# Optimization experiments

Measured on AMD Instinct MI355X. Metric: run time of the kernel, lower is better.

## Reference

```python
import jax, jax.numpy as jnp
import numpy as np

EPS = 1e-7
MIN_NORM = 1e-15
PROJ_EPS = 4e-3
C = 1.0
HEADS = 4
NEG_SLOPE = 0.2

def artanh(x):
    x = jnp.clip(x, -1.0 + EPS, 1.0 - EPS)
    return 0.5 * (jnp.log1p(x) - jnp.log1p(-x))

def _norm(x):
    return jnp.clip(jnp.linalg.norm(x, axis=-1, keepdims=True), MIN_NORM)

def proj(x, c):
    n = _norm(x)
    maxnorm = (1.0 - PROJ_EPS) / jnp.sqrt(c)
    return jnp.where(n > maxnorm, x / n * maxnorm, x)

def expmap0(u, c):
    sc = jnp.sqrt(c)
    n = _norm(u)
    return jnp.tanh(sc * n) * u / (sc * n)

def logmap0(p, c):
    sc = jnp.sqrt(c)
    n = _norm(p)
    return artanh(sc * n) * p / (sc * n)

def mobius_add(x, y, c):
    x2 = jnp.sum(x * x, -1, keepdims=True)
    y2 = jnp.sum(y * y, -1, keepdims=True)
    xy = jnp.sum(x * y, -1, keepdims=True)
    num = (1 + 2 * c * xy + c * y2) * x + (1 - c * x2) * y
    den = 1 + 2 * c * xy + c * c * x2 * y2
    return num / jnp.clip(den, MIN_NORM)

def mobius_matvec(m, x, c):
    sc = jnp.sqrt(c)
    xn = _norm(x)
    mx = x @ m.T
    mxn = _norm(mx)
    res = jnp.tanh(mxn / xn * artanh(sc * xn)) * mx / (mxn * sc)
    zero = jnp.all(mx == 0, axis=-1, keepdims=True)
    return jnp.where(zero, 0.0, res)

def segment_softmax(scores, seg, n):
    # scores: [E, H], seg: [E] destination node ids
    smax = jax.ops.segment_max(scores, seg, num_segments=n)
    smax = jnp.where(jnp.isfinite(smax), smax, 0.0)
    ex = jnp.exp(scores - smax[seg])
    den = jax.ops.segment_sum(ex, seg, num_segments=n)
    return ex / jnp.clip(den[seg], MIN_NORM)


def setup_inputs() -> dict:
    key = jax.random.key(0)
    ks = jax.random.split(key, 6)
    N, D_IN, D_OUT, E = 50000, 128, 128, 800000
    x = 0.01 * jax.random.normal(ks[0], (N, D_IN), dtype=jnp.float32)
    W = (math := np.sqrt(2.0 * 6.0 / (D_IN + D_OUT))) * jax.random.uniform(ks[1], (D_OUT, D_IN), dtype=jnp.float32, minval=-1.0, maxval=1.0)
    lin_bias = jnp.zeros((D_OUT,), jnp.float32)
    att = 0.1 * jax.random.normal(ks[2], (1, HEADS, 2 * (D_OUT // HEADS)), dtype=jnp.float32)
    conv_bias = jnp.zeros((D_OUT,), jnp.float32)
    src = jax.random.randint(ks[3], (E,), 0, N, dtype=jnp.int32)
    # guarantee no self loops (module removes them before adding canonical ones)
    dst = (src + 1 + jax.random.randint(ks[4], (E,), 0, N - 1, dtype=jnp.int32)) % N
    return {"x": x, "W": W, "lin_bias": lin_bias, "att": att,
            "conv_bias": conv_bias, "edge_src": src, "edge_dst": dst}


def reference(x, W, lin_bias, att, conv_bias, edge_src, edge_dst):
    N = x.shape[0]
    H = HEADS
    # ---- HypLinear (c=1, eval mode so no dropout) ----
    h = proj(mobius_matvec(W, x, C), C)
    hyp_bias = proj(expmap0(lin_bias, C), C)   # proj_tan0 is identity on Poincare ball
    h = proj(mobius_add(h, hyp_bias, C), C)
    D = h.shape[-1] // H
    # ---- add self loops ----
    loops = jnp.arange(N, dtype=edge_src.dtype)
    src = jnp.concatenate([edge_src, loops])   # j (source)
    dst = jnp.concatenate([edge_dst, loops])   # i (target / aggregation index)
    # ---- tangent-space GAT message passing ----
    log_x = logmap0(h, C).reshape(N, H, D)
    x_i = log_x[dst]                            # [E, H, D]
    x_j = log_x[src]                            # [E, H, D]
    att_i, att_j = att[0, :, :D], att[0, :, D:]
    alpha = jnp.einsum('ehd,hd->eh', x_i, att_i) + jnp.einsum('ehd,hd->eh', x_j, att_j)
    alpha = jax.nn.leaky_relu(alpha, NEG_SLOPE)
    alpha = segment_softmax(alpha, dst, N)      # [E, H]
    msg = x_j * alpha[:, :, None]
    out = jax.ops.segment_sum(msg, dst, num_segments=N)  # [N, H, D]
    out = out.reshape(N, H * D) + conv_bias
    # ---- update / activation / map back to manifold ----
    out = jax.nn.relu(out)                      # proj_tan0 is identity
    return proj(expmap0(out, C), C)
```

## Files before the change

kernel.cpp:

```cpp
#include <hip/hip_runtime.h>
#include <hip/hip_fp16.h>
#include <math.h>

#define EPSF 1e-7f
#define MIN_NORM 1e-15f
#define MAXNORM 0.996f
#define NEG_SLOPE 0.2f

typedef __attribute__((ext_vector_type(8))) short short8;
typedef __attribute__((ext_vector_type(4))) float f32x4;

__device__ __forceinline__ float wave_reduce_sum(float v) {
    #pragma unroll
    for (int m = 1; m < 64; m <<= 1) v += __shfl_xor(v, m, 64);
    return v;
}

__device__ __forceinline__ float fast_tanh(float x) {
    float e = __expf(2.f * x);
    return 1.f - 2.f / (e + 1.f);
}

__device__ __forceinline__ float fast_artanh(float x) {
    x = fminf(fmaxf(x, -1.f + EPSF), 1.f - EPSF);
    return 0.5f * __logf((1.f + x) / (1.f - x));
}

__device__ __forceinline__ float lrelu(float a) {
    return a < 0.f ? a * NEG_SLOPE : a;
}

__device__ __forceinline__ unsigned short f2bf(float f) {
    unsigned u = __float_as_uint(f);
    u += 0x7FFFu + ((u >> 16) & 1u);
    return (unsigned short)(u >> 16);
}
__device__ __forceinline__ float bf2f(unsigned short h) {
    return __uint_as_float(((unsigned)h) << 16);
}

__global__ void prep_kernel(const float* __restrict__ W,
                            unsigned short* __restrict__ whi,
                            unsigned short* __restrict__ wlo,
                            const float* __restrict__ lin_bias,
                            float* __restrict__ bbuf,
                            int* __restrict__ head, int headN) {
    if (blockIdx.x >= 65) {
        int i = (blockIdx.x - 65) * 1024 + threadIdx.x * 4;
        if (i < headN) *(int4*)&head[i] = make_int4(-1, -1, -1, -1);
        return;
    }
    if (blockIdx.x == 64) {
        if (threadIdx.x >= 64) return;
        int lane = threadIdx.x;
        float u0 = lin_bias[lane], u1 = lin_bias[lane + 64];
        float n2 = wave_reduce_sum(u0 * u0 + u1 * u1);
        float n = fmaxf(sqrtf(n2), MIN_NORM);
        float s = tanhf(n) / n;
        float b0 = s * u0, b1 = s * u1;
        float bn = fmaxf(tanhf(n), MIN_NORM);
        float fn2 = bn * bn;
        if (bn > MAXNORM) { float f = MAXNORM / bn; b0 *= f; b1 *= f; fn2 = MAXNORM * MAXNORM; }
        bbuf[lane] = b0;
        bbuf[lane + 64] = b1;
        if (lane == 0) bbuf[128] = fn2;
        return;
    }
    int idx = blockIdx.x * 256 + threadIdx.x;
    int i = idx & 7, l = (idx >> 3) & 63, ts = idx >> 9;
    int s = ts & 3, t = ts >> 2;
    int o = t * 16 + (l & 15);
    int k = s * 32 + ((l >> 4) * 8) + i;
    float f = W[o * 128 + k];
    unsigned short h = f2bf(f);
    unsigned short lo = f2bf(f - bf2f(h));
    whi[idx] = h;
    wlo[idx] = lo;
}

#define DPAD 132
__global__ __launch_bounds__(256) void node_kernel(
    const float* __restrict__ x,
    const unsigned short* __restrict__ whi, const unsigned short* __restrict__ wlo,
    const float* __restrict__ bbuf, const float* __restrict__ att,
    unsigned short* __restrict__ log_xb,
    float* __restrict__ s_i, float* __restrict__ s_j, int N)
{
    __shared__ float mxs[16][DPAD];
    __shared__ float xn2s[16];
    int tid = threadIdx.x, wave = tid >> 6, lane = tid & 63;
    int nbase = blockIdx.x * 16;
    int arow = lane & 15, kgrp = lane >> 4;
    int anode = min(nbase + arow, N - 1);

    f32x4 acc0 = {0.f, 0.f, 0.f, 0.f};
    f32x4 acc1 = {0.f, 0.f, 0.f, 0.f};
    int t0 = wave * 2, t1 = wave * 2 + 1;
    float x2loc = 0.f;

    #pragma unroll
    for (int s = 0; s < 4; ++s) {
        const float* xp = x + (size_t)anode * 128 + s * 32 + kgrp * 8;
        float4 xa = *(const float4*)xp;
        float4 xb = *(const float4*)(xp + 4);
        float xv[8] = {xa.x, xa.y, xa.z, xa.w, xb.x, xb.y, xb.z, xb.w};
        short8 ahi, alo;
        #pragma unroll
        for (int i = 0; i < 8; ++i) {
            unsigned short h = f2bf(xv[i]);
            unsigned short l = f2bf(xv[i] - bf2f(h));
            ahi[i] = (short)h;
            alo[i] = (short)l;
        }
        if (wave == 0) {
            #pragma unroll
            for (int i = 0; i < 8; ++i) x2loc = fmaf(xv[i], xv[i], x2loc);
        }
        short8 bh0 = *(const short8*)(whi + ((size_t)(t0 * 4 + s) * 64 + lane) * 8);
        short8 bl0 = *(const short8*)(wlo + ((size_t)(t0 * 4 + s) * 64 + lane) * 8);
        short8 bh1 = *(const short8*)(whi + ((size_t)(t1 * 4 + s) * 64 + lane) * 8);
        short8 bl1 = *(const short8*)(wlo + ((size_t)(t1 * 4 + s) * 64 + lane) * 8);
        acc0 = __builtin_amdgcn_mfma_f32_16x16x32_bf16(ahi, bh0, acc0, 0, 0, 0);
        acc0 = __builtin_amdgcn_mfma_f32_16x16x32_bf16(alo, bh0, acc0, 0, 0, 0);
        acc0 = __builtin_amdgcn_mfma_f32_16x16x32_bf16(ahi, bl0, acc0, 0, 0, 0);
        acc1 = __builtin_amdgcn_mfma_f32_16x16x32_bf16(ahi, bh1, acc1, 0, 0, 0);
        acc1 = __builtin_amdgcn_mfma_f32_16x16x32_bf16(alo, bh1, acc1, 0, 0, 0);
        acc1 = __builtin_amdgcn_mfma_f32_16x16x32_bf16(ahi, bl1, acc1, 0, 0, 0);
    }
    if (wave == 0) {
        x2loc += __shfl_xor(x2loc, 16, 64);
        x2loc += __shfl_xor(x2loc, 32, 64);
        if (lane < 16) xn2s[lane] = x2loc;
    }
    #pragma unroll
    for (int r = 0; r < 4; ++r) {
        mxs[kgrp * 4 + r][t0 * 16 + arow] = acc0[r];
        mxs[kgrp * 4 + r][t1 * 16 + arow] = acc1[r];
    }
    __syncthreads();

    int g16 = lane >> 4, l16 = lane & 15;
    int nn = wave * 4 + g16;
    int node = nbase + nn;
    bool valid = node < N;
    int head = l16 >> 2;
    int dbase = l16 * 8;
    int dd8 = (l16 & 3) * 8;
    float bb[8], aiv[8], ajv[8];
    #pragma unroll
    for (int j = 0; j < 8; ++j) {
        bb[j] = bbuf[dbase + j];
        aiv[j] = att[head * 64 + dd8 + j];
        ajv[j] = att[head * 64 + 32 + dd8 + j];
    }
    float y2 = bbuf[128];

    float4 va = *(const float4*)&mxs[nn][dbase];
    float4 vb = *(const float4*)&mxs[nn][dbase + 4];
    float v[8] = {va.x, va.y, va.z, va.w, vb.x, vb.y, vb.z, vb.w};

    float mq = 0.f;
    #pragma unroll
    for (int j = 0; j < 8; ++j) mq = fmaf(v[j], v[j], mq);
    #pragma unroll
    for (int m = 1; m < 16; m <<= 1) mq += __shfl_xor(mq, m, 64);

    float xn2 = xn2s[nn];
    float xn = fmaxf(sqrtf(xn2), MIN_NORM);
    float mxn = fmaxf(sqrtf(mq), MIN_NORM);
    float t = fast_tanh(mxn / xn * fast_artanh(xn));
    float scl = t / mxn;
    bool zero = (mq == 0.f);
    float r[8];
    #pragma unroll
    for (int j = 0; j < 8; ++j) r[j] = zero ? 0.f : scl * v[j];
    float rn2 = zero ? 0.f : t * t;
    float rn = zero ? MIN_NORM : fmaxf(fabsf(t), MIN_NORM);
    float x2 = rn2;
    if (rn > MAXNORM) {
        float f = MAXNORM / rn;
        #pragma unroll
        for (int j = 0; j < 8; ++j) r[j] *= f;
        x2 = MAXNORM * MAXNORM;
    }
    float xy = 0.f;
    #pragma unroll
    for (int j = 0; j < 8; ++j) xy = fmaf(r[j], bb[j], xy);
    #pragma unroll
    for (int m = 1; m < 16; m <<= 1) xy += __shfl_xor(xy, m, 64);
    float cA = 1.f + 2.f * xy + y2;
    float cB = 1.f - x2;
    float dn = fmaxf(1.f + 2.f * xy + x2 * y2, MIN_NORM);
    float inv = 1.f / dn;
    float h[8];
    #pragma unroll
    for (int j = 0; j < 8; ++j) h[j] = (cA * r[j] + cB * bb[j]) * inv;
    float hq = 0.f;
    #pragma unroll
    for (int j = 0; j < 8; ++j) hq = fmaf(h[j], h[j], hq);
    #pragma unroll
    for (int m = 1; m < 16; m <<= 1) hq += __shfl_xor(hq, m, 64);
    float hn = fmaxf(sqrtf(hq), MIN_NORM);
    float ln2 = hq;
    if (hn > MAXNORM) {
        float f = MAXNORM / hn;
        #pragma unroll
        for (int j = 0; j < 8; ++j) h[j] *= f;
        ln2 = MAXNORM * MAXNORM;
    }
    float lnn = fmaxf(sqrtf(ln2), MIN_NORM);
    float ls = fast_artanh(lnn) / lnn;
    float lv[8];
    #pragma unroll
    for (int j = 0; j < 8; ++j) lv[j] = ls * h[j];

    if (valid) {
        uint4 pk;
        pk.x = (unsigned)f2bf(lv[0]) | ((unsigned)f2bf(lv[1]) << 16);
        pk.y = (unsigned)f2bf(lv[2]) | ((unsigned)f2bf(lv[3]) << 16);
        pk.z = (unsigned)f2bf(lv[4]) | ((unsigned)f2bf(lv[5]) << 16);
        pk.w = (unsigned)f2bf(lv[6]) | ((unsigned)f2bf(lv[7]) << 16);
        *(uint4*)&log_xb[(size_t)node * 128 + dbase] = pk;
    }
    float pi = 0.f, pj = 0.f;
    #pragma unroll
    for (int j = 0; j < 8; ++j) {
        pi = fmaf(lv[j], aiv[j], pi);
        pj = fmaf(lv[j], ajv[j], pj);
    }
    pi += __shfl_xor(pi, 1, 64); pi += __shfl_xor(pi, 2, 64);
    pj += __shfl_xor(pj, 1, 64); pj += __shfl_xor(pj, 2, 64);
    if (valid && (l16 & 3) == 0) {
        int pos = ((head & 1) << 1) | (head >> 1);
        s_i[(size_t)node * 4 + pos] = pi;
        s_j[(size_t)node * 4 + pos] = pj;
    }
}

__global__ void buildw_kernel(const int* __restrict__ src, const int* __restrict__ dst,
                              int E, const float* __restrict__ s_i,
                              const float* __restrict__ s_j,
                              int* __restrict__ head, int4* __restrict__ pair16)
{
    int e = blockIdx.x * blockDim.x + threadIdx.x;
    if (e >= E) return;
    int s_ = src[e], d_ = dst[e];
    int prev = atomicExch(&head[(size_t)d_ * 16 + (e & 15)], e);
    float4 si = *(const float4*)(s_i + (size_t)d_ * 4);
    float4 sj = *(const float4*)(s_j + (size_t)s_ * 4);
    float w0 = __expf(lrelu(si.x + sj.x));
    float w1 = __expf(lrelu(si.y + sj.y));
    float w2 = __expf(lrelu(si.z + sj.z));
    float w3 = __expf(lrelu(si.w + sj.w));
    __half2 h01 = __floats2half2_rn(w0, w1);
    __half2 h23 = __floats2half2_rn(w2, w3);
    int4 pr;
    pr.x = s_ << 8;
    pr.y = prev;
    pr.z = *(int*)&h01;
    pr.w = *(int*)&h23;
    pair16[e] = pr;
}

#define MAXS 128
__global__ __launch_bounds__(256) void aggregate_kernel(
    const int* __restrict__ head, const int4* __restrict__ pair16,
    const float* __restrict__ s_i, const float* __restrict__ s_j,
    const unsigned short* __restrict__ log_xb, const float* __restrict__ conv_bias,
    float* __restrict__ out, int N)
{
    __shared__ __align__(16) int slist[4][MAXS];
    __shared__ __align__(16) unsigned wlist[4][MAXS * 2];
    __shared__ int scnt[4];
    int tid = threadIdx.x, wave = tid >> 6, lane = tid & 63;
    int n = blockIdx.x * 4 + wave;
    bool valid = n < N;

    if (lane == 0) scnt[wave] = 0;
    __syncthreads();

    int resume = -1;
    if (valid && lane < 16) {
        int e = head[(size_t)n * 16 + lane];
        while (e >= 0) {
            int4 pr = pair16[e];
            int pos = atomicAdd(&scnt[wave], 1);
            if (pos < MAXS) {
                slist[wave][pos] = pr.x;
                wlist[wave][pos * 2]     = (unsigned)pr.z;
                wlist[wave][pos * 2 + 1] = (unsigned)pr.w;
                e = pr.y;
            } else { resume = e; break; }
        }
    }
    __syncthreads();

    int g = lane >> 5;
    float acc0 = 0.f, acc1 = 0.f, dna = 0.f, dnb = 0.f;

    int deg = 0;
    if (valid) {
        deg = min(scnt[wave], MAXS);
        float2 si2  = *(const float2*)(s_i + (size_t)n * 4 + g * 2);
        float2 sj2n = *(const float2*)(s_j + (size_t)n * 4 + g * 2);
        float ea = __expf(lrelu(si2.x + sj2n.x));
        float eb = __expf(lrelu(si2.y + sj2n.y));
        dna = ea; dnb = eb;
        const unsigned short* mrow = log_xb + (size_t)n * 128;
        acc0 = ea * bf2f(mrow[lane]);
        acc1 = eb * bf2f(mrow[lane + 64]);

        const int* sl = slist[wave];
        const unsigned* wlv = wlist[wave];
        int i = 0;
        for (; i + 8 <= deg; i += 8) {
            int4 offqa = *(const int4*)&sl[i];
            int4 offqb = *(const int4*)&sl[i + 4];
            int offs[8] = {offqa.x, offqa.y, offqa.z, offqa.w,
                           offqb.x, offqb.y, offqb.z, offqb.w};
            unsigned ww[8];
            unsigned short ma[8], mb[8];
            #pragma unroll
            for (int j = 0; j < 8; ++j) {
                ww[j] = wlv[(i + j) * 2 + g];
                const unsigned short* mr =
                    (const unsigned short*)((const char*)log_xb + offs[j]);
                ma[j] = mr[lane];
                mb[j] = mr[lane + 64];
            }
            #pragma unroll
            for (int j = 0; j < 8; ++j) {
                float2 wf = __half22float2(*(const __half2*)&ww[j]);
                dna += wf.x; dnb += wf.y;
                acc0 = fmaf(wf.x, bf2f(ma[j]), acc0);
                acc1 = fmaf(wf.y, bf2f(mb[j]), acc1);
            }
        }
        for (; i + 4 <= deg; i += 4) {
            int4 offq = *(const int4*)&sl[i];
            int offs[4] = {offq.x, offq.y, offq.z, offq.w};
            unsigned ww[4];
            unsigned short ma[4], mb[4];
            #pragma unroll
            for (int j = 0; j < 4; ++j) {
                ww[j] = wlv[(i + j) * 2 + g];
                const unsigned short* mr =
                    (const unsigned short*)((const char*)log_xb + offs[j]);
                ma[j] = mr[lane];
                mb[j] = mr[lane + 64];
            }
            #pragma unroll
            for (int j = 0; j < 4; ++j) {
                float2 wf = __half22float2(*(const __half2*)&ww[j]);
                dna += wf.x; dnb += wf.y;
                acc0 = fmaf(wf.x, bf2f(ma[j]), acc0);
                acc1 = fmaf(wf.y, bf2f(mb[j]), acc1);
            }
        }
        for (; i < deg; ++i) {
            unsigned w = wlv[i * 2 + g];
            const unsigned short* mr =
                (const unsigned short*)((const char*)log_xb + sl[i]);
            float2 wf = __half22float2(*(const __half2*)&w);
            dna += wf.x; dnb += wf.y;
            acc0 = fmaf(wf.x, bf2f(mr[lane]), acc0);
            acc1 = fmaf(wf.y, bf2f(mr[lane + 64]), acc1);
        }
    }

    unsigned long long mask = __ballot(resume >= 0);
    while (mask) {
        int l = __ffsll((long long)mask) - 1;
        int e = __shfl(resume, l, 64);
        while (e >= 0) {
            int off = 0, nx = -1, wz = 0, wwd = 0;
            if (lane == 0) { int4 pr = pair16[e]; off = pr.x; nx = pr.y; wz = pr.z; wwd = pr.w; }
            off = __shfl(off, 0, 64);
            wz = __shfl(wz, 0, 64);
            wwd = __shfl(wwd, 0, 64);
            e = __shfl(nx, 0, 64);
            unsigned wsel = (unsigned)(g ? wwd : wz);
            float2 wf = __half22float2(*(const __half2*)&wsel);
            const unsigned short* mr = (const unsigned short*)((const char*)log_xb + off);
            dna += wf.x; dnb += wf.y;
            acc0 = fmaf(wf.x, bf2f(mr[lane]), acc0);
            acc1 = fmaf(wf.y, bf2f(mr[lane + 64]), acc1);
        }
        mask &= mask - 1;
    }

    if (!valid) return;

    float v0 = acc0 / fmaxf(dna, MIN_NORM) + conv_bias[lane];
    float v1 = acc1 / fmaxf(dnb, MIN_NORM) + conv_bias[lane + 64];
    v0 = fmaxf(v0, 0.f);
    v1 = fmaxf(v1, 0.f);
    float n2 = wave_reduce_sum(v0 * v0 + v1 * v1);
    float nn = fmaxf(sqrtf(n2), MIN_NORM);
    float tv = fast_tanh(nn);
    float s = tv / nn;
    float r0 = s * v0, r1 = s * v1;
    float rn = fmaxf(tv, MIN_NORM);
    if (rn > MAXNORM) { float f = MAXNORM / rn; r0 *= f; r1 *= f; }
    out[(size_t)n * 128 + lane] = r0;
    out[(size_t)n * 128 + 64 + lane] = r1;
}

extern "C" void kernel_launch(void* const* d_in, const int* in_sizes, int n_in,
                              void* d_out, int out_size, void* d_ws, size_t ws_size,
                              hipStream_t stream)
{
    const float* x        = (const float*)d_in[0];
    const float* W        = (const float*)d_in[1];
    const float* lin_bias = (const float*)d_in[2];
    const float* att      = (const float*)d_in[3];
    const float* conv_bias= (const float*)d_in[4];
    const int*   esrc     = (const int*)d_in[5];
    const int*   edst     = (const int*)d_in[6];
    int N = in_sizes[0] / 128;
    int E = in_sizes[5];
    float* out = (float*)d_out;

    char* p = (char*)d_ws;
    float* bbuf   = (float*)p;  p += 256 * 4;
    unsigned short* whi = (unsigned short*)p; p += 16384 * 2;
    unsigned short* wlo = (unsigned short*)p; p += 16384 * 2;
    float* s_i    = (float*)p;  p += (size_t)N * 4 * 4;
    float* s_j    = (float*)p;  p += (size_t)N * 4 * 4;
    int*   head   = (int*)p;    p += (size_t)N * 16 * 4;
    int4*  pair16 = (int4*)p;   p += (size_t)E * 16;
    unsigned short* log_xb = (unsigned short*)p; p += (size_t)N * 128 * 2;

    int headN = N * 16;
    int prepBlocks = 65 + (headN / 4 + 255) / 256;
    prep_kernel<<<prepBlocks, 256, 0, stream>>>(W, whi, wlo, lin_bias, bbuf, head, headN);
    int nTiles = (N + 15) / 16;
    node_kernel<<<nTiles, 256, 0, stream>>>(x, whi, wlo, bbuf, att, log_xb, s_i, s_j, N);
    buildw_kernel<<<(E + 255) / 256, 256, 0, stream>>>(esrc, edst, E, s_i, s_j, head, pair16);
    aggregate_kernel<<<(N + 3) / 4, 256, 0, stream>>>(
        head, pair16, s_i, s_j, log_xb, conv_bias, out, N);
}
```

Baseline: 120.3 us.

## Quantize tangent-space node features to int8 with per-node scale for aggregation

Node features in tangent space are now stored as int8 with a per-node absmax scale instead of bf16. This halves the gather traffic in the aggregation kernel. The scale is carried per edge in a new array, and the attention weight multiplied by the scale is precomputed into shared memory. The cost is an extra per-edge float write and read, a larger shared weight list, and added quantization error that could break tolerance.

```diff
diff --git a/kernel.cpp b/kernel.cpp
--- a/kernel.cpp
+++ b/kernel.cpp
@@ -37,6 +37,10 @@
 }
 __device__ __forceinline__ float bf2f(unsigned short h) {
     return __uint_as_float(((unsigned)h) << 16);
+}
+
+__device__ __forceinline__ unsigned byteof(unsigned x, int k) {
+    return (x >> (8 * k)) & 0xffu;
 }
 
 __global__ void prep_kernel(const float* __restrict__ W,
@@ -83,7 +87,7 @@
     const float* __restrict__ x,
     const unsigned short* __restrict__ whi, const unsigned short* __restrict__ wlo,
     const float* __restrict__ bbuf, const float* __restrict__ att,
-    unsigned short* __restrict__ log_xb,
+    unsigned short* __restrict__ logq, float* __restrict__ scl,
     float* __restrict__ s_i, float* __restrict__ s_j, int N)
 {
     __shared__ float mxs[16][DPAD];
@@ -169,11 +173,11 @@
     float xn = fmaxf(sqrtf(xn2), MIN_NORM);
     float mxn = fmaxf(sqrtf(mq), MIN_NORM);
     float t = fast_tanh(mxn / xn * fast_artanh(xn));
-    float scl = t / mxn;
+    float scl_ = t / mxn;
     bool zero = (mq == 0.f);
     float r[8];
     #pragma unroll
-    for (int j = 0; j < 8; ++j) r[j] = zero ? 0.f : scl * v[j];
+    for (int j = 0; j < 8; ++j) r[j] = zero ? 0.f : scl_ * v[j];
     float rn2 = zero ? 0.f : t * t;
     float rn = zero ? MIN_NORM : fmaxf(fabsf(t), MIN_NORM);
     float x2 = rn2;
@@ -214,14 +218,30 @@
     #pragma unroll
     for (int j = 0; j < 8; ++j) lv[j] = ls * h[j];
 
-    if (valid) {
+    float rm = 0.f;
+    #pragma unroll
+    for (int j = 0; j < 8; ++j) rm = fmaxf(rm, fabsf(lv[j]));
+    #pragma unroll
+    for (int m = 1; m < 16; m <<= 1) rm = fmaxf(rm, __shfl_xor(rm, m, 64));
+    float s127 = rm * (1.f / 127.f);
+    float qs = rm > 0.f ? 127.f / rm : 0.f;
+    int q[8];
+    #pragma unroll
+    for (int j = 0; j < 8; ++j) q[j] = (int)rintf(lv[j] * qs);
+    unsigned o0 = (q[0] & 255) | ((q[1] & 255) << 8) | ((q[2] & 255) << 16) | ((unsigned)(q[3] & 255) << 24);
+    unsigned o1 = (q[4] & 255) | ((q[5] & 255) << 8) | ((q[6] & 255) << 16) | ((unsigned)(q[7] & 255) << 24);
+    unsigned p0 = __shfl_xor(o0, 8, 64);
+    unsigned p1 = __shfl_xor(o1, 8, 64);
+    if (valid && l16 < 8) {
         uint4 pk;
-        pk.x = (unsigned)f2bf(lv[0]) | ((unsigned)f2bf(lv[1]) << 16);
-        pk.y = (unsigned)f2bf(lv[2]) | ((unsigned)f2bf(lv[3]) << 16);
-        pk.z = (unsigned)f2bf(lv[4]) | ((unsigned)f2bf(lv[5]) << 16);
-        pk.w = (unsigned)f2bf(lv[6]) | ((unsigned)f2bf(lv[7]) << 16);
-        *(uint4*)&log_xb[(size_t)node * 128 + dbase] = pk;
-    }
+        pk.x = byteof(o0,0) | (byteof(p0,0) << 8) | (byteof(o0,1) << 16) | (byteof(p0,1) << 24);
+        pk.y = byteof(o0,2) | (byteof(p0,2) << 8) | (byteof(o0,3) << 16) | (byteof(p0,3) << 24);
+        pk.z = byteof(o1,0) | (byteof(p1,0) << 8) | (byteof(o1,1) << 16) | (byteof(p1,1) << 24);
+        pk.w = byteof(o1,2) | (byteof(p1,2) << 8) | (byteof(o1,3) << 16) | (byteof(p1,3) << 24);
+        *(uint4*)((char*)logq + ((size_t)node << 7) + l16 * 16) = pk;
+    }
+    if (valid && l16 == 0) scl[node] = s127;
+
     float pi = 0.f, pj = 0.f;
     #pragma unroll
     for (int j = 0; j < 8; ++j) {
@@ -239,8 +259,9 @@
 
 __global__ void buildw_kernel(const int* __restrict__ src, const int* __restrict__ dst,
                               int E, const float* __restrict__ s_i,
-                              const float* __restrict__ s_j,
-                              int* __restrict__ head, int4* __restrict__ pair16)
+                              const float* __restrict__ s_j, const float* __restrict__ scl,
+                              int* __restrict__ head, int4* __restrict__ pair16,
+                              float* __restrict__ sacc)
 {
     int e = blockIdx.x * blockDim.x + threadIdx.x;
     if (e >= E) return;
@@ -248,6 +269,7 @@
     int prev = atomicExch(&head[(size_t)d_ * 16 + (e & 15)], e);
     float4 si = *(const float4*)(s_i + (size_t)d_ * 4);
     float4 sj = *(const float4*)(s_j + (size_t)s_ * 4);
+    float sa = scl[s_];
     float w0 = __expf(lrelu(si.x + sj.x));
     float w1 = __expf(lrelu(si.y + sj.y));
     float w2 = __expf(lrelu(si.z + sj.z));
@@ -255,22 +277,25 @@
     __half2 h01 = __floats2half2_rn(w0, w1);
     __half2 h23 = __floats2half2_rn(w2, w3);
     int4 pr;
-    pr.x = s_ << 8;
+    pr.x = s_ << 7;
     pr.y = prev;
     pr.z = *(int*)&h01;
     pr.w = *(int*)&h23;
     pair16[e] = pr;
+    sacc[e] = sa;
 }
 
 #define MAXS 128
 __global__ __launch_bounds__(256) void aggregate_kernel(
     const int* __restrict__ head, const int4* __restrict__ pair16,
+    const float* __restrict__ sacc,
     const float* __restrict__ s_i, const float* __restrict__ s_j,
-    const unsigned short* __restrict__ log_xb, const float* __restrict__ conv_bias,
+    const float* __restrict__ scl,
+    const unsigned short* __restrict__ logq, const float* __restrict__ conv_bias,
     float* __restrict__ out, int N)
 {
     __shared__ __align__(16) int slist[4][MAXS];
-    __shared__ __align__(16) unsigned wlist[4][MAXS * 2];
+    __shared__ __align__(16) unsigned wlist[4][MAXS * 4];
     __shared__ int scnt[4];
     int tid = threadIdx.x, wave = tid >> 6, lane = tid & 63;
     int n = blockIdx.x * 4 + wave;
@@ -284,11 +309,18 @@
         int e = head[(size_t)n * 16 + lane];
         while (e >= 0) {
             int4 pr = pair16[e];
+            float sa = sacc[e];
             int pos = atomicAdd(&scnt[wave], 1);
             if (pos < MAXS) {
+                float2 f01 = __half22float2(*(const __half2*)&pr.z);
+                float2 f23 = __half22float2(*(const __half2*)&pr.w);
+                __half2 a01 = __floats2half2_rn(f01.x * sa, f01.y * sa);
+                __half2 a23 = __floats2half2_rn(f23.x * sa, f23.y * sa);
                 slist[wave][pos] = pr.x;
-                wlist[wave][pos * 2]     = (unsigned)pr.z;
-                wlist[wave][pos * 2 + 1] = (unsigned)pr.w;
+                wlist[wave][pos * 4 + 0] = (unsigned)pr.z;
+                wlist[wave][pos * 4 + 1] = (unsigned)pr.w;
+                wlist[wave][pos * 4 + 2] = *(unsigned*)&a01;
+                wlist[wave][pos * 4 + 3] = *(unsigned*)&a23;
                 e = pr.y;
             } else { resume = e; break; }
         }
@@ -297,18 +329,23 @@
 
     int g = lane >> 5;
     float acc0 = 0.f, acc1 = 0.f, dna = 0.f, dnb = 0.f;
+    float sia = 0.f, sib = 0.f;
 
     int deg = 0;
     if (valid) {
         deg = min(scnt[wave], MAXS);
         float2 si2  = *(const float2*)(s_i + (size_t)n * 4 + g * 2);
         float2 sj2n = *(const float2*)(s_j + (size_t)n * 4 + g * 2);
-        float ea = __expf(lrelu(si2.x + sj2n.x));
-        float eb = __expf(lrelu(si2.y + sj2n.y));
+        sia = si2.x; sib = si2.y;
+        float ea = __expf(lrelu(sia + sj2n.x));
+        float eb = __expf(lrelu(sib + sj2n.y));
         dna = ea; dnb = eb;
-        const unsigned short* mrow = log_xb + (size_t)n * 128;
-        acc0 = ea * bf2f(mrow[lane]);
-        acc1 = eb * bf2f(mrow[lane + 64]);
+        float sn = scl[n];
+        unsigned short us = *(const unsigned short*)((const char*)logq + ((size_t)n << 7) + lane * 2);
+        int q0s = (signed char)(us & 0xff);
+        int q1s = (signed char)(us >> 8);
+        acc0 = (ea * sn) * (float)q0s;
+        acc1 = (eb * sn) * (float)q1s;
 
         const int* sl = slist[wave];
         const unsigned* wlv = wlist[wave];
@@ -318,53 +355,58 @@
             int4 offqb = *(const int4*)&sl[i + 4];
             int offs[8] = {offqa.x, offqa.y, offqa.z, offqa.w,
                            offqb.x, offqb.y, offqb.z, offqb.w};
-            unsigned ww[8];
-            unsigned short ma[8], mb[8];
+            unsigned wd[8], wa[8];
+            unsigned short uu[8];
             #pragma unroll
             for (int j = 0; j < 8; ++j) {
-                ww[j] = wlv[(i + j) * 2 + g];
-                const unsigned short* mr =
-                    (const unsigned short*)((const char*)log_xb + offs[j]);
-                ma[j] = mr[lane];
-                mb[j] = mr[lane + 64];
+                wd[j] = wlv[(i + j) * 4 + g];
+                wa[j] = wlv[(i + j) * 4 + 2 + g];
+                uu[j] = *(const unsigned short*)((const char*)logq + offs[j] + lane * 2);
             }
             #pragma unroll
             for (int j = 0; j < 8; ++j) {
-                float2 wf = __half22float2(*(const __half2*)&ww[j]);
+                float2 wf = __half22float2(*(const __half2*)&wd[j]);
+                float2 af = __half22float2(*(const __half2*)&wa[j]);
+                int q0 = (signed char)(uu[j] & 0xff);
+                int q1 = (signed char)(uu[j] >> 8);
                 dna += wf.x; dnb += wf.y;
-                acc0 = fmaf(wf.x, bf2f(ma[j]), acc0);
-                acc1 = fmaf(wf.y, bf2f(mb[j]), acc1);
+                acc0 = fmaf(af.x, (float)q0, acc0);
+                acc1 = fmaf(af.y, (float)q1, acc1);
             }
         }
         for (; i + 4 <= deg; i += 4) {
             int4 offq = *(const int4*)&sl[i];
             int offs[4] = {offq.x, offq.y, offq.z, offq.w};
-            unsigned ww[4];
-            unsigned short ma[4], mb[4];
+            unsigned wd[4], wa[4];
+            unsigned short uu[4];
             #pragma unroll
             for (int j = 0; j < 4; ++j) {
-                ww[j] = wlv[(i + j) * 2 + g];
-                const unsigned short* mr =
-                    (const unsigned short*)((const char*)log_xb + offs[j]);
-                ma[j] = mr[lane];
-                mb[j] = mr[lane + 64];
+                wd[j] = wlv[(i + j) * 4 + g];
+                wa[j] = wlv[(i + j) * 4 + 2 + g];
+                uu[j] = *(const unsigned short*)((const char*)logq + offs[j] + lane * 2);
             }
             #pragma unroll
             for (int j = 0; j < 4; ++j) {
-                float2 wf = __half22float2(*(const __half2*)&ww[j]);
+                float2 wf = __half22float2(*(const __half2*)&wd[j]);
+                float2 af = __half22float2(*(const __half2*)&wa[j]);
+                int q0 = (signed char)(uu[j] & 0xff);
+                int q1 = (signed char)(uu[j] >> 8);
                 dna += wf.x; dnb += wf.y;
-                acc0 = fmaf(wf.x, bf2f(ma[j]), acc0);
-                acc1 = fmaf(wf.y, bf2f(mb[j]), acc1);
+                acc0 = fmaf(af.x, (float)q0, acc0);
+                acc1 = fmaf(af.y, (float)q1, acc1);
             }
         }
         for (; i < deg; ++i) {
-            unsigned w = wlv[i * 2 + g];
-            const unsigned short* mr =
-                (const unsigned short*)((const char*)log_xb + sl[i]);
-            float2 wf = __half22float2(*(const __half2*)&w);
+            unsigned wd = wlv[i * 4 + g];
+            unsigned wa = wlv[i * 4 + 2 + g];
+            unsigned short uu = *(const unsigned short*)((const char*)logq + sl[i] + lane * 2);
+            float2 wf = __half22float2(*(const __half2*)&wd);
+            float2 af = __half22float2(*(const __half2*)&wa);
+            int q0 = (signed char)(uu & 0xff);
+            int q1 = (signed char)(uu >> 8);
             dna += wf.x; dnb += wf.y;
-            acc0 = fmaf(wf.x, bf2f(mr[lane]), acc0);
-            acc1 = fmaf(wf.y, bf2f(mr[lane + 64]), acc1);
+            acc0 = fmaf(af.x, (float)q0, acc0);
+            acc1 = fmaf(af.y, (float)q1, acc1);
         }
     }
 
@@ -374,17 +416,25 @@
         int e = __shfl(resume, l, 64);
         while (e >= 0) {
             int off = 0, nx = -1, wz = 0, wwd = 0;
-            if (lane == 0) { int4 pr = pair16[e]; off = pr.x; nx = pr.y; wz = pr.z; wwd = pr.w; }
+            float sa = 0.f;
+            if (lane == 0) {
+                int4 pr = pair16[e];
+                off = pr.x; nx = pr.y; wz = pr.z; wwd = pr.w;
+                sa = sacc[e];
+            }
             off = __shfl(off, 0, 64);
             wz = __shfl(wz, 0, 64);
             wwd = __shfl(wwd, 0, 64);
+            sa = __shfl(sa, 0, 64);
             e = __shfl(nx, 0, 64);
             unsigned wsel = (unsigned)(g ? wwd : wz);
             float2 wf = __half22float2(*(const __half2*)&wsel);
-            const unsigned short* mr = (const unsigned short*)((const char*)log_xb + off);
+            unsigned short uu = *(const unsigned short*)((const char*)logq + off + lane * 2);
+            int q0 = (signed char)(uu & 0xff);
+            int q1 = (signed char)(uu >> 8);
             dna += wf.x; dnb += wf.y;
-            acc0 = fmaf(wf.x, bf2f(mr[lane]), acc0);
-            acc1 = fmaf(wf.y, bf2f(mr[lane + 64]), acc1);
+            acc0 = fmaf(wf.x * sa, (float)q0, acc0);
+            acc1 = fmaf(wf.y * sa, (float)q1, acc1);
         }
         mask &= mask - 1;
     }
@@ -427,16 +477,19 @@
     unsigned short* wlo = (unsigned short*)p; p += 16384 * 2;
     float* s_i    = (float*)p;  p += (size_t)N * 4 * 4;
     float* s_j    = (float*)p;  p += (size_t)N * 4 * 4;
+    float* scl    = (float*)p;  p += (size_t)N * 4;
     int*   head   = (int*)p;    p += (size_t)N * 16 * 4;
     int4*  pair16 = (int4*)p;   p += (size_t)E * 16;
-    unsigned short* log_xb = (unsigned short*)p; p += (size_t)N * 128 * 2;
+    float* sacc   = (float*)p;  p += (size_t)E * 4;
+    unsigned short* logq = (unsigned short*)p; p += (size_t)N * 64 * 2;
 
     int headN = N * 16;
     int prepBlocks = 65 + (headN / 4 + 255) / 256;
     prep_kernel<<<prepBlocks, 256, 0, stream>>>(W, whi, wlo, lin_bias, bbuf, head, headN);
     int nTiles = (N + 15) / 16;
-    node_kernel<<<nTiles, 256, 0, stream>>>(x, whi, wlo, bbuf, att, log_xb, s_i, s_j, N);
-    buildw_kernel<<<(E + 255) / 256, 256, 0, stream>>>(esrc, edst, E, s_i, s_j, head, pair16);
+    node_kernel<<<nTiles, 256, 0, stream>>>(x, whi, wlo, bbuf, att, logq, scl, s_i, s_j, N);
+    buildw_kernel<<<(E + 255) / 256, 256, 0, stream>>>(esrc, edst, E, s_i, s_j, scl,
+                                                       head, pair16, sacc);
     aggregate_kernel<<<(N + 3) / 4, 256, 0, stream>>>(
-        head, pair16, s_i, s_j, log_xb, conv_bias, out, N);
-}
+        head, pair16, sacc, s_i, s_j, scl, logq, conv_bias, out, N);
+}
```

Measured after the change: 126.5 us. +5.2%, slower.
